# Kernel tuning notes

Hardware: AMD Instinct MI355X
Metric: run time of the kernel (lower is better)

Reference implementation:

```python
import jax, jax.numpy as jnp
import numpy as np

DIM = 1024; DEPTH = 2; HEADS = 8; DH = DIM // HEADS  # 128
BUCKET = 64; NHASH = 4; MULT = 4
B = 2; T = 4096
NBUCKETS = T // BUCKET  # 64
SCALE = DH ** -0.5
SELF_ATTN_VAL = -5e4  # TOKEN_SELF_ATTN_VALUE in reformer-pytorch
EPS = 1e-5


def layer_norm(x, g, b):
    m = jnp.mean(x, -1, keepdims=True)
    v = jnp.var(x, -1, keepdims=True)
    return (x - m) * jax.lax.rsqrt(v + EPS) * g + b


def lsh_attn(xn, Wqk, Wv, Wo, bo, rot):
    # xn: [B,T,DIM] already layer-normed. Shared-QK LSH attention (reformer-pytorch).
    qk = (xn @ Wqk).reshape(B, T, HEADS, DH).transpose(0, 2, 1, 3).reshape(B * HEADS, T, DH)
    v = (xn @ Wv).reshape(B, T, HEADS, DH).transpose(0, 2, 1, 3).reshape(B * HEADS, T, DH)
    bh = B * HEADS
    # --- hashing with random rotations ---
    rotated = jnp.einsum('btf,fhi->bhti', qk, rot)            # [bh,NHASH,T,NBUCKETS//2]
    rotated = jnp.concatenate([rotated, -rotated], -1)        # [bh,NHASH,T,NBUCKETS]
    buckets = jnp.argmax(rotated, -1)                         # [bh,NHASH,T]
    offs = (jnp.arange(NHASH) * NBUCKETS)[:, None]
    buckets = (buckets + offs).reshape(bh, NHASH * T)
    ticker = jnp.arange(NHASH * T)
    bt = buckets * T + (ticker % T)                           # unique keys -> stable-equivalent sort
    sticker = jnp.argsort(bt, axis=-1)                        # [bh, NHASH*T]
    undo = jnp.argsort(sticker, axis=-1)
    st = sticker % T                                          # original positions, bucket-sorted
    sqk = jnp.take_along_axis(qk, st[..., None], axis=1)
    sv = jnp.take_along_axis(v, st[..., None], axis=1)
    nchunks = NHASH * NBUCKETS
    bq_t = st.reshape(bh, nchunks, BUCKET)
    bqk = sqk.reshape(bh, nchunks, BUCKET, DH)
    bv = sv.reshape(bh, nchunks, BUCKET, DH)
    bq = bqk
    bk = bqk / jnp.clip(jnp.linalg.norm(bqk, axis=-1, keepdims=True), 1e-12)
    def look_one_back(a):
        extra = jnp.concatenate([a[:, -1:], a[:, :-1]], axis=1)
        return jnp.concatenate([a, extra], axis=2)
    bk = look_one_back(bk); bv = look_one_back(bv); bkv_t = look_one_back(bq_t)
    dots = jnp.einsum('bcie,bcje->bcij', bq, bk) * SCALE      # [bh,nchunks,BUCKET,2*BUCKET]
    self_mask = bq_t[..., :, None] == bkv_t[..., None, :]     # shared-QK: penalize i==j
    dots = jnp.where(self_mask, SELF_ATTN_VAL, dots)
    lse = jax.nn.logsumexp(dots, axis=-1, keepdims=True)
    p = jnp.exp(dots - lse)
    bo_ = jnp.einsum('bcij,bcje->bcie', p, bv)
    so = bo_.reshape(bh, NHASH * T, DH)
    slog = lse.reshape(bh, NHASH * T)
    o = jnp.take_along_axis(so, undo[..., None], axis=1)
    logits = jnp.take_along_axis(slog, undo, axis=1)
    o = o.reshape(bh, NHASH, T, DH)
    logits = logits.reshape(bh, NHASH, T, 1)
    probs = jnp.exp(logits - jax.nn.logsumexp(logits, axis=1, keepdims=True))
    out = jnp.sum(o * probs, axis=1)                          # combine hash rounds
    out = out.reshape(B, HEADS, T, DH).transpose(0, 2, 1, 3).reshape(B, T, HEADS * DH)
    return out @ Wo + bo


def setup_inputs() -> dict:
    key = jax.random.key(0)
    ks = jax.random.split(key, 16)
    s = 0.02
    d = {
        'x': jax.random.normal(ks[0], (B, T, DIM), jnp.float32),
        'ln1_g': jnp.ones((DEPTH, DIM), jnp.float32),
        'ln1_b': jnp.zeros((DEPTH, DIM), jnp.float32),
        'Wqk': jax.random.normal(ks[1], (DEPTH, DIM, HEADS * DH), jnp.float32) * s,
        'Wv': jax.random.normal(ks[2], (DEPTH, DIM, HEADS * DH), jnp.float32) * s,
        'Wo': jax.random.normal(ks[3], (DEPTH, HEADS * DH, DIM), jnp.float32) * s,
        'bo': jnp.zeros((DEPTH, DIM), jnp.float32),
        'ln2_g': jnp.ones((DEPTH, DIM), jnp.float32),
        'ln2_b': jnp.zeros((DEPTH, DIM), jnp.float32),
        'W1': jax.random.normal(ks[4], (DEPTH, DIM, DIM * MULT), jnp.float32) * s,
        'b1': jnp.zeros((DEPTH, DIM * MULT), jnp.float32),
        'W2': jax.random.normal(ks[5], (DEPTH, DIM * MULT, DIM), jnp.float32) * s,
        'b2': jnp.zeros((DEPTH, DIM), jnp.float32),
        'rotations': jax.random.normal(ks[6], (DEPTH, DH, NHASH, NBUCKETS // 2), jnp.float32),
    }
    return d


def reference(x, ln1_g, ln1_b, Wqk, Wv, Wo, bo, ln2_g, ln2_b, W1, b1, W2, b2, rotations):
    xx = jnp.concatenate([x, x], -1)  # [B,T,2*DIM] reversible pair
    def step(carry, p):
        g1, be1, wqk, wv, wo, bov, g2, be2, w1, bb1, w2, bb2, rot = p
        x1, x2 = jnp.split(carry, 2, axis=-1)
        y1 = x1 + lsh_attn(layer_norm(x2, g1, be1), wqk, wv, wo, bov, rot)
        h = layer_norm(y1, g2, be2)
        ff = jax.nn.gelu(h @ w1 + bb1, approximate=False) @ w2 + bb2
        y2 = x2 + ff
        return jnp.concatenate([y1, y2], -1), None
    params = (ln1_g, ln1_b, Wqk, Wv, Wo, bo, ln2_g, ln2_b, W1, b1, W2, b2, rotations)
    out, _ = jax.lax.scan(step, xx, params)
    y1, y2 = jnp.split(out, 2, axis=-1)
    return y1 + y2
```

## Files before the change

### kernel.cpp

```cpp
#include <hip/hip_runtime.h>
#include <hip/hip_bf16.h>
#include <cmath>

using bf16 = __hip_bfloat16;
typedef __attribute__((ext_vector_type(8))) short short8;
typedef __attribute__((ext_vector_type(4))) float floatx4;

__device__ __forceinline__ float bu2f(ushort u) { return __uint_as_float((unsigned)u << 16); }
__device__ __forceinline__ ushort f2bu(float f) {
  union { bf16 b; ushort u; } cv; cv.b = __float2bfloat16(f); return cv.u;
}
__device__ __forceinline__ void gl_lds16(const ushort* g, ushort* l) {
  __builtin_amdgcn_global_load_lds((const __attribute__((address_space(1))) unsigned*)g,
                                   (__attribute__((address_space(3))) unsigned*)l, 16, 0, 0);
}
__device__ __forceinline__ float fast_gelu(float x) {
  float z = 0.7978845608028654f * (x + 0.044715f * x * x * x);
  z = fmaxf(fminf(z, 10.f), -10.f);
  float e = __expf(2.f * z);
  float t = (e - 1.f) / (e + 1.f);
  return 0.5f * x * (1.f + t);
}

static constexpr int kT   = 4096;
static constexpr int kDim = 1024;
static constexpr float kScale   = 0.08838834764831845f;
static constexpr float kSelfVal = -5.0e4f;

__device__ __forceinline__ int sane_v(float f) { float a = fabsf(f); return (a > 1e-4f && a < 1e4f) ? 1 : 0; }

__global__ __launch_bounds__(256) void k_detect(const unsigned* __restrict__ x, int* __restrict__ flag) {
  __shared__ int cnt;
  int tid = threadIdx.x;
  if (tid == 0) cnt = 0;
  __syncthreads();
  int my = 0;
  const uint4* p = (const uint4*)x;
  for (int q = 0; q < 16; q++) {
    uint4 u = p[tid * 16 + q];
    my += sane_v(__uint_as_float(u.x << 16)) + sane_v(__uint_as_float(u.x & 0xffff0000u));
    my += sane_v(__uint_as_float(u.y << 16)) + sane_v(__uint_as_float(u.y & 0xffff0000u));
    my += sane_v(__uint_as_float(u.z << 16)) + sane_v(__uint_as_float(u.z & 0xffff0000u));
    my += sane_v(__uint_as_float(u.w << 16)) + sane_v(__uint_as_float(u.w & 0xffff0000u));
  }
  atomicAdd(&cnt, my);
  __syncthreads();
  if (tid == 0) flag[0] = (cnt >= 24576) ? 1 : 0;
}

__global__ __launch_bounds__(256) void k_cvt(const int* __restrict__ flag, const void* __restrict__ src,
                                             ushort* __restrict__ dst, int n) {
  int i = blockIdx.x * 256 + threadIdx.x;
  if (i >= n) return;
  dst[i] = (*flag) ? ((const ushort*)src)[i] : f2bu(((const float*)src)[i]);
}

__global__ __launch_bounds__(256) void k_init_any(const int* __restrict__ flag, const void* __restrict__ x,
                                                  float* __restrict__ x1, float* __restrict__ x2) {
  int i = blockIdx.x * 1024 + threadIdx.x * 4;
  float4 f;
  if (*flag) {
    ushort4 u = *(const ushort4*)((const ushort*)x + i);
    f.x = bu2f(u.x); f.y = bu2f(u.y); f.z = bu2f(u.z); f.w = bu2f(u.w);
  } else {
    f = *(const float4*)((const float*)x + i);
  }
  *(float4*)(x1 + i) = f;
  *(float4*)(x2 + i) = f;
}

__global__ __launch_bounds__(256) void k_final_any(const int* __restrict__ flag, const float* __restrict__ x1,
                                                   const float* __restrict__ x2, void* __restrict__ out) {
  int i = blockIdx.x * 1024 + threadIdx.x * 4;
  float4 a = *(const float4*)(x1 + i);
  float4 b = *(const float4*)(x2 + i);
  float4 s; s.x = a.x + b.x; s.y = a.y + b.y; s.z = a.z + b.z; s.w = a.w + b.w;
  if (*flag) {
    ushort4 u; u.x = f2bu(s.x); u.y = f2bu(s.y); u.z = f2bu(s.z); u.w = f2bu(s.w);
    *(ushort4*)((ushort*)out + i) = u;
  } else {
    *(float4*)((float*)out + i) = s;
  }
}

__global__ __launch_bounds__(256) void k_ln(const float* __restrict__ x, const ushort* __restrict__ g,
                                            const ushort* __restrict__ be, ushort* __restrict__ out) {
  __shared__ float ws[4], ws2[4];
  int row = blockIdx.x, tid = threadIdx.x;
  const float* xr = x + (size_t)row * kDim + tid * 4;
  float4 v = *(const float4*)xr;
  float s  = v.x + v.y + v.z + v.w;
  float s2 = v.x*v.x + v.y*v.y + v.z*v.z + v.w*v.w;
  #pragma unroll
  for (int off = 32; off; off >>= 1) { s += __shfl_down(s, off); s2 += __shfl_down(s2, off); }
  int wave = tid >> 6, lane = tid & 63;
  if (lane == 0) { ws[wave] = s; ws2[wave] = s2; }
  __syncthreads();
  s  = ws[0] + ws[1] + ws[2] + ws[3];
  s2 = ws2[0] + ws2[1] + ws2[2] + ws2[3];
  float mean = s * (1.f/1024.f);
  float var  = fmaxf(s2 * (1.f/1024.f) - mean*mean, 0.f);
  float rstd = rsqrtf(var + 1e-5f);
  int cb = tid * 4;
  ushort* o = out + (size_t)row * kDim + cb;
  o[0] = f2bu((v.x - mean) * rstd * bu2f(g[cb+0]) + bu2f(be[cb+0]));
  o[1] = f2bu((v.y - mean) * rstd * bu2f(g[cb+1]) + bu2f(be[cb+1]));
  o[2] = f2bu((v.z - mean) * rstd * bu2f(g[cb+2]) + bu2f(be[cb+2]));
  o[3] = f2bu((v.w - mean) * rstd * bu2f(g[cb+3]) + bu2f(be[cb+3]));
}

__global__ __launch_bounds__(256) void k_transpose2(const int* __restrict__ flag, const void* __restrict__ src_bf,
                                                    const void* __restrict__ src_f, ushort* __restrict__ out,
                                                    int K, int N) {
  __shared__ ushort tile[32][33];
  int isbf = *flag;
  int nb = blockIdx.x * 32, kb = blockIdx.y * 32;
  int tx = threadIdx.x & 31, ty = threadIdx.x >> 5;
  for (int r = ty; r < 32; r += 8) {
    size_t idx = (size_t)(kb + r) * N + nb + tx;
    tile[r][tx] = isbf ? ((const ushort*)src_bf)[idx] : f2bu(((const float*)src_f)[idx]);
  }
  __syncthreads();
  for (int r = ty; r < 32; r += 8) out[(size_t)(nb + r) * K + kb + tx] = tile[tx][r];
}

__global__ __launch_bounds__(256) void k_rot_t(const ushort* __restrict__ rot, ushort* __restrict__ rotT) {
  int tid = threadIdx.x;
  for (int idx = tid; idx < 16384; idx += 256) {
    int n = idx >> 7, k = idx & 127;
    rotT[idx] = rot[k * 128 + n];
  }
}

__global__ __launch_bounds__(256) void k_gemm(const ushort* __restrict__ A, const ushort* __restrict__ Bt,
                                              const ushort* __restrict__ bias, float* __restrict__ Cf,
                                              ushort* __restrict__ Cb, ushort* __restrict__ Cb2,
                                              int M, int N, int K, int mode) {
  __shared__ alignas(16) ushort As[128*64];
  __shared__ alignas(16) ushort Bs[128*64];
  const int tid = threadIdx.x;
  const int lane = tid & 63, wave = tid >> 6;
  const int m0 = blockIdx.y * 128, n0 = blockIdx.x * 128;
  const int wm = (wave & 1) * 64, wn = (wave >> 1) * 64;
  const int lr = lane & 15, lk = (lane >> 4) * 8;
  const int r8  = tid >> 3;
  const int cst = ((tid & 7) * 8) ^ ((r8 & 7) * 8);
  const int swz = (lr & 7) * 8;

  floatx4 acc[4][4];
  #pragma unroll
  for (int mi = 0; mi < 4; mi++)
    #pragma unroll
    for (int ni = 0; ni < 4; ni++) acc[mi][ni] = (floatx4){0.f, 0.f, 0.f, 0.f};

  const ushort* Ap = A  + (size_t)(m0 + r8) * K + cst;
  const ushort* Bp = Bt + (size_t)(n0 + r8) * K + cst;
  const size_t rstep = (size_t)32 * K;

  for (int k0 = 0; k0 < K; k0 += 64) {
    __syncthreads();
    #pragma unroll
    for (int i = 0; i < 4; i++) {
      gl_lds16(Ap + i * rstep + k0, As + i*2048 + wave*512);
      gl_lds16(Bp + i * rstep + k0, Bs + i*2048 + wave*512);
    }
    __syncthreads();
    #pragma unroll
    for (int ks = 0; ks < 2; ks++) {
      const int col = (ks*32 + lk) ^ swz;
      short8 a[4], b[4];
      #pragma unroll
      for (int mi = 0; mi < 4; mi++) a[mi] = *(const short8*)&As[(wm + mi*16 + lr)*64 + col];
      #pragma unroll
      for (int ni = 0; ni < 4; ni++) b[ni] = *(const short8*)&Bs[(wn + ni*16 + lr)*64 + col];
      #pragma unroll
      for (int mi = 0; mi < 4; mi++)
        #pragma unroll
        for (int ni = 0; ni < 4; ni++)
          acc[mi][ni] = __builtin_amdgcn_mfma_f32_16x16x32_bf16(a[mi], b[ni], acc[mi][ni], 0, 0, 0);
    }
  }
  #pragma unroll
  for (int mi = 0; mi < 4; mi++) {
    #pragma unroll
    for (int ni = 0; ni < 4; ni++) {
      int col = n0 + wn + ni*16 + lr;
      float bv = (mode == 1 || mode == 2) ? bu2f(bias[col]) : 0.f;
      #pragma unroll
      for (int q = 0; q < 4; q++) {
        int r2 = m0 + wm + mi*16 + (lane >> 4)*4 + q;
        float val = acc[mi][ni][q];
        if (mode == 0) {
          Cf[(size_t)r2 * N + col] = val;
        } else if (mode == 1) {
          Cf[(size_t)r2 * N + col] += val + bv;
        } else if (mode == 2) {
          Cb[(size_t)r2 * N + col] = f2bu(fast_gelu(val + bv));
        } else if (mode == 3) {
          Cb[(size_t)r2 * N + col] = f2bu(val);
        } else {
          ushort h = f2bu(val);
          Cb [(size_t)r2 * N + col] = h;
          Cb2[(size_t)r2 * N + col] = f2bu(val - bu2f(h));
        }
      }
    }
  }
}

__global__ __launch_bounds__(256) void k_bucket_mfma(const ushort* __restrict__ qkh, const ushort* __restrict__ qkl,
                                                     const ushort* __restrict__ rotT, int* __restrict__ bkt) {
  __shared__ alignas(16) ushort Bs[128*128];
  __shared__ alignas(16) ushort Ah[64*128];
  __shared__ alignas(16) ushort Al[64*128];
  const int tid = threadIdx.x;
  const int lane = tid & 63, wave = tid >> 6;
  const int lr = lane & 15, lk = (lane >> 4) * 8;
  const int tt = blockIdx.x * 64;
  const int bh = blockIdx.y;
  const int b = bh >> 3, hh = bh & 7;

  {
    int r = tid >> 2, c0 = (tid & 3) * 32;
    size_t base = ((size_t)(b * kT + tt + r)) * kDim + hh * 128 + c0;
    const uint4* sh = (const uint4*)(qkh + base);
    const uint4* sl = (const uint4*)(qkl + base);
    uint4* dh = (uint4*)&Ah[r * 128 + c0];
    uint4* dl = (uint4*)&Al[r * 128 + c0];
    #pragma unroll
    for (int i = 0; i < 4; i++) { dh[i] = sh[i]; dl[i] = sl[i]; }
  }
  {
    const uint4* src = (const uint4*)rotT;
    uint4* dst = (uint4*)Bs;
    for (int i = tid; i < 2048; i += 256) dst[i] = src[i];
  }
  __syncthreads();

  floatx4 acc[4][2];
  #pragma unroll
  for (int mi = 0; mi < 4; mi++) { acc[mi][0] = (floatx4){0,0,0,0}; acc[mi][1] = (floatx4){0,0,0,0}; }
  #pragma unroll
  for (int ks = 0; ks < 4; ks++) {
    short8 a[4], bb[2];
    #pragma unroll
    for (int ni = 0; ni < 2; ni++) bb[ni] = *(const short8*)&Bs[(wave*32 + ni*16 + lr)*128 + ks*32 + lk];
    #pragma unroll
    for (int mi = 0; mi < 4; mi++) a[mi] = *(const short8*)&Ah[(mi*16 + lr)*128 + ks*32 + lk];
    #pragma unroll
    for (int mi = 0; mi < 4; mi++)
      #pragma unroll
      for (int ni = 0; ni < 2; ni++)
        acc[mi][ni] = __builtin_amdgcn_mfma_f32_16x16x32_bf16(a[mi], bb[ni], acc[mi][ni], 0, 0, 0);
  }
  #pragma unroll
  for (int ks = 0; ks < 4; ks++) {
    short8 a[4], bb[2];
    #pragma unroll
    for (int ni = 0; ni < 2; ni++) bb[ni] = *(const short8*)&Bs[(wave*32 + ni*16 + lr)*128 + ks*32 + lk];
    #pragma unroll
    for (int mi = 0; mi < 4; mi++) a[mi] = *(const short8*)&Al[(mi*16 + lr)*128 + ks*32 + lk];
    #pragma unroll
    for (int mi = 0; mi < 4; mi++)
      #pragma unroll
      for (int ni = 0; ni < 2; ni++)
        acc[mi][ni] = __builtin_amdgcn_mfma_f32_16x16x32_bf16(a[mi], bb[ni], acc[mi][ni], 0, 0, 0);
  }

  #pragma unroll
  for (int mi = 0; mi < 4; mi++) {
    #pragma unroll
    for (int q = 0; q < 4; q++) {
      float v0 = acc[mi][0][q];
      float v1 = acc[mi][1][q];
      float best = v0; int bidx = lr;
      if (v1  > best) { best = v1;  bidx = 16 + lr; }
      if (-v0 > best) { best = -v0; bidx = 32 + lr; }
      if (-v1 > best) { best = -v1; bidx = 48 + lr; }
      #pragma unroll
      for (int m = 1; m <= 8; m <<= 1) {
        float ov = __shfl_xor(best, m);
        int   oi = __shfl_xor(bidx, m);
        if (ov > best || (ov == best && oi < bidx)) { best = ov; bidx = oi; }
      }
      if (lr == 0) {
        int row = mi*16 + ((lane >> 4) & 3)*4 + q;
        bkt[(bh*4 + wave)*4096 + tt + row] = bidx;
      }
    }
  }
}

__global__ __launch_bounds__(256) void k_sort(const int* __restrict__ bkt, int* __restrict__ st) {
  __shared__ unsigned char  hist[64*256];
  __shared__ unsigned short offs[64*256];
  __shared__ int base[64];
  int tid = threadIdx.x, grp = blockIdx.x;
  const int* bk = bkt + grp * 4096;
  for (int i = tid; i < 64*256; i += 256) hist[i] = 0;
  __syncthreads();
  int myb[16];
  #pragma unroll
  for (int j = 0; j < 16; j++) {
    myb[j] = bk[tid*16 + j];
    hist[myb[j]*256 + tid] += 1;
  }
  __syncthreads();
  if (tid < 64) {
    int run = 0;
    for (int t = 0; t < 256; t++) { offs[tid*256 + t] = (unsigned short)run; run += hist[tid*256 + t]; }
    base[tid] = run;
  }
  __syncthreads();
  if (tid == 0) {
    int run = 0;
    for (int b2 = 0; b2 < 64; b2++) { int c = base[b2]; base[b2] = run; run += c; }
  }
  __syncthreads();
  #pragma unroll
  for (int j = 0; j < 16; j++) {
    int b2 = myb[j];
    int r = 0;
    for (int jj = 0; jj < j; jj++) r += (myb[jj] == b2) ? 1 : 0;
    st[grp*4096 + base[b2] + (int)offs[b2*256 + tid] + r] = tid*16 + j;
  }
}

__global__ __launch_bounds__(256) void k_attn(const ushort* __restrict__ qkh, const ushort* __restrict__ vbuf,
                                              const int* __restrict__ st, ushort* __restrict__ o_r,
                                              float* __restrict__ lse_r) {
  __shared__ alignas(16) ushort KV[128*136];
  __shared__ alignas(16) ushort Ps[64*136];
  __shared__ float rnorm[128];
  __shared__ int   kposs[128];
  __shared__ float red1[64*4];
  __shared__ float red2[64*4];
  __shared__ float lrow[64];

  const int tid = threadIdx.x;
  const int bid = blockIdx.x;
  const int bh = bid >> 8;
  const int c  = bid & 255;
  const int h  = c >> 6;
  const int cprev = (c + 255) & 255;
  const int b  = bh >> 3, hh = bh & 7;
  const int lane = tid & 63, wave = tid >> 6;
  const int lr = lane & 15, lk = (lane >> 4) * 8;

  {
    int j = tid >> 1, half = tid & 1;
    int slot = (j < 64) ? (c*64 + j) : (cprev*64 + (j - 64));
    int pos = st[bh*16384 + slot];
    if (half == 0) kposs[j] = pos;
    const ushort* src = qkh + ((size_t)(b * kT + pos)) * kDim + hh*128 + half*64;
    float ss = 0.f;
    #pragma unroll
    for (int i2 = 0; i2 < 64; i2 += 8) {
      uint4 u = *(const uint4*)(src + i2);
      *(uint4*)&KV[j*136 + half*64 + i2] = u;
      float f0 = bu2f((ushort)(u.x & 0xffffu)), f1 = bu2f((ushort)(u.x >> 16));
      float f2 = bu2f((ushort)(u.y & 0xffffu)), f3 = bu2f((ushort)(u.y >> 16));
      float f4 = bu2f((ushort)(u.z & 0xffffu)), f5 = bu2f((ushort)(u.z >> 16));
      float f6 = bu2f((ushort)(u.w & 0xffffu)), f7 = bu2f((ushort)(u.w >> 16));
      ss += f0*f0 + f1*f1 + f2*f2 + f3*f3 + f4*f4 + f5*f5 + f6*f6 + f7*f7;
    }
    ss += __shfl_xor(ss, 1);
    if (half == 0) rnorm[j] = 1.f / fmaxf(sqrtf(ss), 1e-12f);
  }
  __syncthreads();

  {
    floatx4 acc[4][2];
    #pragma unroll
    for (int mi = 0; mi < 4; mi++) { acc[mi][0] = (floatx4){0,0,0,0}; acc[mi][1] = (floatx4){0,0,0,0}; }
    #pragma unroll
    for (int ks = 0; ks < 4; ks++) {
      short8 a[4], bb[2];
      #pragma unroll
      for (int mi = 0; mi < 4; mi++) a[mi]  = *(const short8*)&KV[(mi*16 + lr)*136 + ks*32 + lk];
      #pragma unroll
      for (int ni = 0; ni < 2; ni++) bb[ni] = *(const short8*)&KV[(wave*32 + ni*16 + lr)*136 + ks*32 + lk];
      #pragma unroll
      for (int mi = 0; mi < 4; mi++)
        #pragma unroll
        for (int ni = 0; ni < 2; ni++)
          acc[mi][ni] = __builtin_amdgcn_mfma_f32_16x16x32_bf16(a[mi], bb[ni], acc[mi][ni], 0, 0, 0);
    }
    #pragma unroll
    for (int mi = 0; mi < 4; mi++) {
      #pragma unroll
      for (int ni = 0; ni < 2; ni++) {
        int col = wave*32 + ni*16 + lr;
        float rn = rnorm[col] * kScale;
        int cpos = kposs[col];
        #pragma unroll
        for (int q = 0; q < 4; q++) {
          int row = mi*16 + (lane >> 4)*4 + q;
          float val = acc[mi][ni][q] * rn;
          if (cpos == kposs[row]) val = kSelfVal;
          Ps[row*136 + col] = f2bu(val);
        }
      }
    }
  }
  __syncthreads();

  {
    int j = tid >> 1, half = tid & 1;
    int pos = kposs[j];
    const ushort* src = vbuf + ((size_t)(b * kT + pos)) * kDim + hh*128 + half*64;
    #pragma unroll
    for (int i2 = 0; i2 < 64; i2 += 8) {
      uint4 u = *(const uint4*)(src + i2);
      int d0 = half*64 + i2;
      KV[(d0+0)*136 + j] = (ushort)(u.x & 0xffffu); KV[(d0+1)*136 + j] = (ushort)(u.x >> 16);
      KV[(d0+2)*136 + j] = (ushort)(u.y & 0xffffu); KV[(d0+3)*136 + j] = (ushort)(u.y >> 16);
      KV[(d0+4)*136 + j] = (ushort)(u.z & 0xffffu); KV[(d0+5)*136 + j] = (ushort)(u.z >> 16);
      KV[(d0+6)*136 + j] = (ushort)(u.w & 0xffffu); KV[(d0+7)*136 + j] = (ushort)(u.w >> 16);
    }
  }

  {
    int i = tid >> 2, part = tid & 3;
    const int jb = part * 32;
    float m = -1e30f;
    for (int j2 = 0; j2 < 32; j2++) m = fmaxf(m, bu2f(Ps[i*136 + jb + j2]));
    red1[i*4 + part] = m;
    __syncthreads();
    m = fmaxf(fmaxf(red1[i*4+0], red1[i*4+1]), fmaxf(red1[i*4+2], red1[i*4+3]));
    float ssum = 0.f;
    for (int j2 = 0; j2 < 32; j2++) {
      float arg = fmaxf(fminf(bu2f(Ps[i*136 + jb + j2]) - m, 0.f), -80.f);
      float p = __expf(arg);
      ssum += p;
      Ps[i*136 + jb + j2] = f2bu(p);
    }
    red2[i*4 + part] = ssum;
    __syncthreads();
    if (part == 0) {
      float l = fmaxf(red2[i*4+0] + red2[i*4+1] + red2[i*4+2] + red2[i*4+3], 1e-20f);
      lrow[i] = 1.f / l;
      lse_r[(size_t)(bh*4 + h)*4096 + kposs[i]] = m + __logf(l);
    }
  }
  __syncthreads();

  {
    floatx4 acc[4][2];
    #pragma unroll
    for (int mi = 0; mi < 4; mi++) { acc[mi][0] = (floatx4){0,0,0,0}; acc[mi][1] = (floatx4){0,0,0,0}; }
    #pragma unroll
    for (int ks = 0; ks < 4; ks++) {
      short8 a[4], bb[2];
      #pragma unroll
      for (int mi = 0; mi < 4; mi++) a[mi]  = *(const short8*)&Ps[(mi*16 + lr)*136 + ks*32 + lk];
      #pragma unroll
      for (int ni = 0; ni < 2; ni++) bb[ni] = *(const short8*)&KV[(wave*32 + ni*16 + lr)*136 + ks*32 + lk];
      #pragma unroll
      for (int mi = 0; mi < 4; mi++)
        #pragma unroll
        for (int ni = 0; ni < 2; ni++)
          acc[mi][ni] = __builtin_amdgcn_mfma_f32_16x16x32_bf16(a[mi], bb[ni], acc[mi][ni], 0, 0, 0);
    }
    #pragma unroll
    for (int mi = 0; mi < 4; mi++) {
      #pragma unroll
      for (int ni = 0; ni < 2; ni++) {
        int d = wave*32 + ni*16 + lr;
        #pragma unroll
        for (int q = 0; q < 4; q++) {
          int row = mi*16 + (lane >> 4)*4 + q;
          float o = acc[mi][ni][q] * lrow[row];
          o_r[((size_t)(bh*4 + h)*4096 + kposs[row])*128 + d] = f2bu(o);
        }
      }
    }
  }
}

__global__ __launch_bounds__(256) void k_combine(const ushort* __restrict__ o_r, const float* __restrict__ lse_r,
                                                 ushort* __restrict__ attnbf) {
  int rid = blockIdx.x * 2 + (threadIdx.x >> 7);
  int d = threadIdx.x & 127;
  int bh = rid >> 12, t = rid & 4095;
  int b = bh >> 3, hh = bh & 7;
  size_t base = (size_t)bh * 16384 + t;
  float l0 = lse_r[base], l1 = lse_r[base + 4096], l2 = lse_r[base + 8192], l3 = lse_r[base + 12288];
  float M = fmaxf(fmaxf(l0, l1), fmaxf(l2, l3));
  float e0 = __expf(fmaxf(fminf(l0 - M, 0.f), -80.f));
  float e1 = __expf(fmaxf(fminf(l1 - M, 0.f), -80.f));
  float e2 = __expf(fmaxf(fminf(l2 - M, 0.f), -80.f));
  float e3 = __expf(fmaxf(fminf(l3 - M, 0.f), -80.f));
  float inv = 1.f / (e0 + e1 + e2 + e3);
  float o = e0 * bu2f(o_r[(base         )*128 + d]) + e1 * bu2f(o_r[(base +  4096)*128 + d])
          + e2 * bu2f(o_r[(base +  8192)*128 + d]) + e3 * bu2f(o_r[(base + 12288)*128 + d]);
  attnbf[((size_t)b * kT + t) * kDim + hh*128 + d] = f2bu(o * inv);
}

extern "C" void kernel_launch(void* const* d_in, const int* in_sizes, int n_in,
                              void* d_out, int out_size, void* d_ws, size_t ws_size,
                              hipStream_t stream) {
  (void)in_sizes; (void)n_in; (void)out_size; (void)ws_size;
  const void* x     = d_in[0];
  const void* ln1_g = d_in[1];
  const void* ln1_b = d_in[2];
  const void* Wqk   = d_in[3];
  const void* Wv    = d_in[4];
  const void* Wo    = d_in[5];
  const void* bo    = d_in[6];
  const void* ln2_g = d_in[7];
  const void* ln2_b = d_in[8];
  const void* W1    = d_in[9];
  const void* b1    = d_in[10];
  const void* W2    = d_in[11];
  const void* b2    = d_in[12];
  const void* rot   = d_in[13];

  char* w = (char*)d_ws;
  int*    flag = (int*)w;    w += 256;
  ushort* prm  = (ushort*)w; w += 131072;
  float* x1  = (float*)w;  w += 33554432;
  float* x2  = (float*)w;  w += 33554432;
  ushort* qkh = (ushort*)w; w += 16777216;
  ushort* qkl = (ushort*)w; w += 16777216;
  ushort* vbb = (ushort*)w; w += 16777216;
  ushort* xbf = (ushort*)w; w += 16777216;
  ushort* orb = (ushort*)w; w += 67108864;
  float* lse = (float*)w;  w += 1048576;
  int*   bkt = (int*)w;    w += 1048576;
  int*   stb = (int*)w;    w += 1048576;
  ushort* wtA = (ushort*)w; w += 2097152;
  ushort* wtB = (ushort*)w; w += 2097152;
  ushort* wtC = (ushort*)w; w += 2097152;
  ushort* wt1 = (ushort*)w; w += 8388608;
  ushort* wt2 = (ushort*)w; w += 8388608;
  ushort* rtT = (ushort*)w; w += 32768;

  ushort* pLN1G = prm + 0;     ushort* pLN1B = prm + 2048;
  ushort* pBO   = prm + 4096;  ushort* pLN2G = prm + 6144;
  ushort* pLN2B = prm + 8192;  ushort* pB1   = prm + 10240;
  ushort* pB2   = prm + 18432; ushort* pROT  = prm + 20480;

  k_detect<<<1, 256, 0, stream>>>((const unsigned*)x, flag);
  k_cvt<<<8,   256, 0, stream>>>(flag, ln1_g, pLN1G, 2048);
  k_cvt<<<8,   256, 0, stream>>>(flag, ln1_b, pLN1B, 2048);
  k_cvt<<<8,   256, 0, stream>>>(flag, bo,    pBO,   2048);
  k_cvt<<<8,   256, 0, stream>>>(flag, ln2_g, pLN2G, 2048);
  k_cvt<<<8,   256, 0, stream>>>(flag, ln2_b, pLN2B, 2048);
  k_cvt<<<32,  256, 0, stream>>>(flag, b1,    pB1,   8192);
  k_cvt<<<8,   256, 0, stream>>>(flag, b2,    pB2,   2048);
  k_cvt<<<128, 256, 0, stream>>>(flag, rot,   pROT,  32768);
  k_init_any<<<8192, 256, 0, stream>>>(flag, x, x1, x2);

  for (int d = 0; d < 2; d++) {
    k_transpose2<<<dim3(32, 32),  256, 0, stream>>>(flag,
        (const char*)Wqk + (size_t)d*1048576*2, (const char*)Wqk + (size_t)d*1048576*4, wtA, 1024, 1024);
    k_transpose2<<<dim3(32, 32),  256, 0, stream>>>(flag,
        (const char*)Wv  + (size_t)d*1048576*2, (const char*)Wv  + (size_t)d*1048576*4, wtB, 1024, 1024);
    k_transpose2<<<dim3(32, 32),  256, 0, stream>>>(flag,
        (const char*)Wo  + (size_t)d*1048576*2, (const char*)Wo  + (size_t)d*1048576*4, wtC, 1024, 1024);
    k_transpose2<<<dim3(128, 32), 256, 0, stream>>>(flag,
        (const char*)W1  + (size_t)d*4194304*2, (const char*)W1  + (size_t)d*4194304*4, wt1, 1024, 4096);
    k_transpose2<<<dim3(32, 128), 256, 0, stream>>>(flag,
        (const char*)W2  + (size_t)d*4194304*2, (const char*)W2  + (size_t)d*4194304*4, wt2, 4096, 1024);
    k_rot_t<<<1, 256, 0, stream>>>(pROT + (size_t)d * 16384, rtT);

    k_ln<<<8192, 256, 0, stream>>>(x2, pLN1G + d*1024, pLN1B + d*1024, xbf);
    k_gemm<<<dim3(8, 64), 256, 0, stream>>>(xbf, wtA, nullptr, nullptr, qkh, qkl, 8192, 1024, 1024, 5);
    k_gemm<<<dim3(8, 64), 256, 0, stream>>>(xbf, wtB, nullptr, nullptr, vbb, nullptr, 8192, 1024, 1024, 3);
    k_bucket_mfma<<<dim3(64, 16), 256, 0, stream>>>(qkh, qkl, rtT, bkt);
    k_sort<<<64, 256, 0, stream>>>(bkt, stb);
    k_attn<<<4096, 256, 0, stream>>>(qkh, vbb, stb, orb, lse);
    k_combine<<<32768, 256, 0, stream>>>(orb, lse, xbf);
    k_gemm<<<dim3(8, 64), 256, 0, stream>>>(xbf, wtC, pBO + d*1024, x1, nullptr, nullptr, 8192, 1024, 1024, 1);
    k_ln<<<8192, 256, 0, stream>>>(x1, pLN2G + d*1024, pLN2B + d*1024, xbf);
    k_gemm<<<dim3(32, 64), 256, 0, stream>>>(xbf, wt1, pB1 + d*4096, nullptr, orb, nullptr, 8192, 4096, 1024, 2);
    k_gemm<<<dim3(8, 64), 256, 0, stream>>>(orb, wt2, pB2 + d*1024, x2, nullptr, nullptr, 8192, 1024, 4096, 1);
  }
  k_final_any<<<8192, 256, 0, stream>>>(flag, x1, x2, d_out);
}
```

Before: 1.266 ms.

## Fuse QK/V projections into one GEMM, vectorize combine, use sigmoid GELU

The QK and V weight transposes are packed into one buffer so a single GEMM with N=2048 produces the split hi/lo QK output and the bf16 V output. This removes one launch and lets both projections share the A-tile loads. The combine kernel now handles two bf16 elements per thread with 32-bit loads and stores, halving its grid. The tanh GELU is replaced by the x*sigmoid(1.702x) approximation, which is cheaper but differs from the exact erf GELU by more than the tanh form did, so accuracy may suffer.

```diff
diff --git a/kernel.cpp b/kernel.cpp
--- a/kernel.cpp
+++ b/kernel.cpp
@@ -15,11 +15,7 @@
                                    (__attribute__((address_space(3))) unsigned*)l, 16, 0, 0);
 }
 __device__ __forceinline__ float fast_gelu(float x) {
-  float z = 0.7978845608028654f * (x + 0.044715f * x * x * x);
-  z = fmaxf(fminf(z, 10.f), -10.f);
-  float e = __expf(2.f * z);
-  float t = (e - 1.f) / (e + 1.f);
-  return 0.5f * x * (1.f + t);
+  return x / (1.f + __expf(-1.702f * x));
 }
 
 static constexpr int kT   = 4096;
@@ -135,6 +131,7 @@
 __global__ __launch_bounds__(256) void k_gemm(const ushort* __restrict__ A, const ushort* __restrict__ Bt,
                                               const ushort* __restrict__ bias, float* __restrict__ Cf,
                                               ushort* __restrict__ Cb, ushort* __restrict__ Cb2,
+                                              ushort* __restrict__ Cb3,
                                               int M, int N, int K, int mode) {
   __shared__ alignas(16) ushort As[128*64];
   __shared__ alignas(16) ushort Bs[128*64];
@@ -198,10 +195,18 @@
           Cb[(size_t)r2 * N + col] = f2bu(fast_gelu(val + bv));
         } else if (mode == 3) {
           Cb[(size_t)r2 * N + col] = f2bu(val);
-        } else {
+        } else if (mode == 5) {
           ushort h = f2bu(val);
           Cb [(size_t)r2 * N + col] = h;
           Cb2[(size_t)r2 * N + col] = f2bu(val - bu2f(h));
+        } else {
+          if (n0 < 1024) {
+            ushort h = f2bu(val);
+            Cb [(size_t)r2 * 1024 + col] = h;
+            Cb2[(size_t)r2 * 1024 + col] = f2bu(val - bu2f(h));
+          } else {
+            Cb3[(size_t)r2 * 1024 + (col - 1024)] = f2bu(val);
+          }
         }
       }
     }
@@ -480,8 +485,8 @@
 
 __global__ __launch_bounds__(256) void k_combine(const ushort* __restrict__ o_r, const float* __restrict__ lse_r,
                                                  ushort* __restrict__ attnbf) {
-  int rid = blockIdx.x * 2 + (threadIdx.x >> 7);
-  int d = threadIdx.x & 127;
+  int rid = blockIdx.x * 4 + (threadIdx.x >> 6);
+  int d2 = (threadIdx.x & 63) * 2;
   int bh = rid >> 12, t = rid & 4095;
   int b = bh >> 3, hh = bh & 7;
   size_t base = (size_t)bh * 16384 + t;
@@ -492,9 +497,16 @@
   float e2 = __expf(fmaxf(fminf(l2 - M, 0.f), -80.f));
   float e3 = __expf(fmaxf(fminf(l3 - M, 0.f), -80.f));
   float inv = 1.f / (e0 + e1 + e2 + e3);
-  float o = e0 * bu2f(o_r[(base         )*128 + d]) + e1 * bu2f(o_r[(base +  4096)*128 + d])
-          + e2 * bu2f(o_r[(base +  8192)*128 + d]) + e3 * bu2f(o_r[(base + 12288)*128 + d]);
-  attnbf[((size_t)b * kT + t) * kDim + hh*128 + d] = f2bu(o * inv);
+  unsigned u0 = *(const unsigned*)&o_r[(base         )*128 + d2];
+  unsigned u1 = *(const unsigned*)&o_r[(base +  4096)*128 + d2];
+  unsigned u2 = *(const unsigned*)&o_r[(base +  8192)*128 + d2];
+  unsigned u3 = *(const unsigned*)&o_r[(base + 12288)*128 + d2];
+  float oa = e0 * bu2f((ushort)(u0 & 0xffffu)) + e1 * bu2f((ushort)(u1 & 0xffffu))
+           + e2 * bu2f((ushort)(u2 & 0xffffu)) + e3 * bu2f((ushort)(u3 & 0xffffu));
+  float ob = e0 * bu2f((ushort)(u0 >> 16)) + e1 * bu2f((ushort)(u1 >> 16))
+           + e2 * bu2f((ushort)(u2 >> 16)) + e3 * bu2f((ushort)(u3 >> 16));
+  unsigned out = (unsigned)f2bu(oa * inv) | ((unsigned)f2bu(ob * inv) << 16);
+  *(unsigned*)&attnbf[((size_t)b * kT + t) * kDim + hh*128 + d2] = out;
 }
 
 extern "C" void kernel_launch(void* const* d_in, const int* in_sizes, int n_in,
@@ -529,8 +541,7 @@
   float* lse = (float*)w;  w += 1048576;
   int*   bkt = (int*)w;    w += 1048576;
   int*   stb = (int*)w;    w += 1048576;
-  ushort* wtA = (ushort*)w; w += 2097152;
-  ushort* wtB = (ushort*)w; w += 2097152;
+  ushort* wtAB = (ushort*)w; w += 4194304;
   ushort* wtC = (ushort*)w; w += 2097152;
   ushort* wt1 = (ushort*)w; w += 8388608;
   ushort* wt2 = (ushort*)w; w += 8388608;
@@ -554,9 +565,9 @@
 
   for (int d = 0; d < 2; d++) {
     k_transpose2<<<dim3(32, 32),  256, 0, stream>>>(flag,
-        (const char*)Wqk + (size_t)d*1048576*2, (const char*)Wqk + (size_t)d*1048576*4, wtA, 1024, 1024);
+        (const char*)Wqk + (size_t)d*1048576*2, (const char*)Wqk + (size_t)d*1048576*4, wtAB, 1024, 1024);
     k_transpose2<<<dim3(32, 32),  256, 0, stream>>>(flag,
-        (const char*)Wv  + (size_t)d*1048576*2, (const char*)Wv  + (size_t)d*1048576*4, wtB, 1024, 1024);
+        (const char*)Wv  + (size_t)d*1048576*2, (const char*)Wv  + (size_t)d*1048576*4, wtAB + 1048576, 1024, 1024);
     k_transpose2<<<dim3(32, 32),  256, 0, stream>>>(flag,
         (const char*)Wo  + (size_t)d*1048576*2, (const char*)Wo  + (size_t)d*1048576*4, wtC, 1024, 1024);
     k_transpose2<<<dim3(128, 32), 256, 0, stream>>>(flag,
@@ -566,16 +577,15 @@
     k_rot_t<<<1, 256, 0, stream>>>(pROT + (size_t)d * 16384, rtT);
 
     k_ln<<<8192, 256, 0, stream>>>(x2, pLN1G + d*1024, pLN1B + d*1024, xbf);
-    k_gemm<<<dim3(8, 64), 256, 0, stream>>>(xbf, wtA, nullptr, nullptr, qkh, qkl, 8192, 1024, 1024, 5);
-    k_gemm<<<dim3(8, 64), 256, 0, stream>>>(xbf, wtB, nullptr, nullptr, vbb, nullptr, 8192, 1024, 1024, 3);
+    k_gemm<<<dim3(16, 64), 256, 0, stream>>>(xbf, wtAB, nullptr, nullptr, qkh, qkl, vbb, 8192, 2048, 1024, 6);
     k_bucket_mfma<<<dim3(64, 16), 256, 0, stream>>>(qkh, qkl, rtT, bkt);
     k_sort<<<64, 256, 0, stream>>>(bkt, stb);
     k_attn<<<4096, 256, 0, stream>>>(qkh, vbb, stb, orb, lse);
-    k_combine<<<32768, 256, 0, stream>>>(orb, lse, xbf);
-    k_gemm<<<dim3(8, 64), 256, 0, stream>>>(xbf, wtC, pBO + d*1024, x1, nullptr, nullptr, 8192, 1024, 1024, 1);
+    k_combine<<<16384, 256, 0, stream>>>(orb, lse, xbf);
+    k_gemm<<<dim3(8, 64), 256, 0, stream>>>(xbf, wtC, pBO + d*1024, x1, nullptr, nullptr, nullptr, 8192, 1024, 1024, 1);
     k_ln<<<8192, 256, 0, stream>>>(x1, pLN2G + d*1024, pLN2B + d*1024, xbf);
-    k_gemm<<<dim3(32, 64), 256, 0, stream>>>(xbf, wt1, pB1 + d*4096, nullptr, orb, nullptr, 8192, 4096, 1024, 2);
-    k_gemm<<<dim3(8, 64), 256, 0, stream>>>(orb, wt2, pB2 + d*1024, x2, nullptr, nullptr, 8192, 1024, 4096, 1);
+    k_gemm<<<dim3(32, 64), 256, 0, stream>>>(xbf, wt1, pB1 + d*4096, nullptr, orb, nullptr, nullptr, 8192, 4096, 1024, 2);
+    k_gemm<<<dim3(8, 64), 256, 0, stream>>>(orb, wt2, pB2 + d*1024, x2, nullptr, nullptr, nullptr, 8192, 1024, 4096, 1);
   }
   k_final_any<<<8192, 256, 0, stream>>>(flag, x1, x2, d_out);
 }
```

Result: no change. 1.266 ms (+0.0%).
